# Kernel tuning notes

Hardware: AMD Instinct MI355X
Metric: run time of the kernel (lower is better)

The kernel has to match this reference:

```python
import jax, jax.numpy as jnp
import numpy as np

# ---------- filter construction (setup-time, numpy) ----------

def _conv2full(A, B):
    out = np.zeros((A.shape[0] + B.shape[0] - 1, A.shape[1] + B.shape[1] - 1))
    for i in range(B.shape[0]):
        for j in range(B.shape[1]):
            out[i:i + A.shape[0], j:j + A.shape[1]] += B[i, j] * A
    return out

def _mctrans(b, t):
    # McClellan transform of 1-D zero-phase filter b through kernel t
    n = (len(b) - 1) // 2
    c = len(b) // 2
    a = np.concatenate([[b[c]], 2.0 * b[c + 1:]])
    P0 = np.array([[1.0]]); P1 = t
    h = a[1] * t
    h[t.shape[0] // 2, t.shape[1] // 2] += a[0]
    for i in range(2, n + 1):
        P2 = 2.0 * _conv2full(t, P1)
        off = ((P2.shape[0] - P0.shape[0]) // 2, (P2.shape[1] - P0.shape[1]) // 2)
        P2[off[0]:off[0] + P0.shape[0], off[1]:off[1] + P0.shape[1]] -= P0
        hn = a[i] * P2
        o2 = ((P2.shape[0] - h.shape[0]) // 2, (P2.shape[1] - h.shape[1]) // 2)
        hn[o2[0]:o2[0] + h.shape[0], o2[1]:o2[1] + h.shape[1]] += h
        h = hn; P0, P1 = P1, P2
    return h

def _make_filters():
    # pyramidal 'maxflat' 1-D analysis pair (pfilters-style), DC gain sqrt(2)
    k1 = 1.0 - np.sqrt(2.0); k2 = 1.0 / np.sqrt(2.0); k3 = k1; M1 = 1.0 / np.sqrt(2.0)
    hh = np.array([0.25 * k2 * k3, 0.5 * k2, 1.0 + 0.5 * k2 * k3]) * M1
    h = np.concatenate([hh, hh[-2::-1]]) * np.sqrt(2.0)          # 5 taps
    gg = np.array([-0.125 * k1 * k2 * k3, 0.25 * k1 * k2,
                   -0.5 * k1 - 0.5 * k3 - 0.375 * k1 * k2 * k3,
                   1.0 + 0.5 * k1 * k2]) * M1
    g = np.concatenate([gg, gg[-2::-1]]) * np.sqrt(2.0)          # 7 taps
    # diamond maxflat lowpass via McClellan transform of Lagrange halfband
    b = np.array([-1., 0., 9., 16., 9., 0., -1.]) / 32.0
    t = np.array([[0., .25, 0.], [.25, 0., .25], [0., .25, 0.]])
    d0 = _mctrans(b, t)                                           # 7x7 diamond LP
    kh, kw = d0.shape
    mm = (-1.0) ** (np.add.outer(np.arange(kh) - kh // 2, np.arange(kw) - kw // 2))
    d1 = d0 * mm                                                  # complementary diamond
    colmod = (-1.0) ** (np.arange(kw) - kw // 2)                  # diamond -> fan
    f0 = d0 * colmod * np.sqrt(2.0)
    f1 = d1 * colmod * np.sqrt(2.0)
    return h, g, f0, f1

# ---------- jax filtering / resampling primitives ----------

def _sepfilt_per(x, f):
    # separable zero-phase filtering with periodic extension; x [B,C,H,W]
    B, C, H, W = x.shape
    L = f.shape[0]; p = L // 2
    k = f.astype(x.dtype)
    y = jnp.pad(x, ((0, 0), (0, 0), (p, p), (0, 0)), mode='wrap').reshape(B * C, 1, H + 2 * p, W)
    y = jax.lax.conv_general_dilated(y, k.reshape(1, 1, L, 1), (1, 1), 'VALID')
    y = jnp.pad(y, ((0, 0), (0, 0), (0, 0), (p, p)), mode='wrap')
    y = jax.lax.conv_general_dilated(y, k.reshape(1, 1, 1, L), (1, 1), 'VALID')
    return y.reshape(B, C, H, W)

def _filt2_per(x, F):
    B, C, H, W = x.shape
    kh, kw = F.shape; ph, pw = kh // 2, kw // 2
    y = jnp.pad(x, ((0, 0), (0, 0), (ph, ph), (pw, pw)), mode='wrap').reshape(B * C, 1, H + 2 * ph, W + 2 * pw)
    y = jax.lax.conv_general_dilated(y, F.reshape(1, 1, kh, kw).astype(x.dtype), (1, 1), 'VALID')
    return y.reshape(B, C, H, W)

def _qdown_r(x):
    # quincunx downsample: periodic row-shear then keep even rows -> [.., H/2, W]
    H, W = x.shape[-2], x.shape[-1]
    idx = (jnp.arange(W)[None, :] + jnp.arange(H)[:, None]) % W
    z = jnp.take_along_axis(x, jnp.broadcast_to(idx, x.shape), axis=-1)
    return z[..., ::2, :]

def _qdown_c(x):
    # quincunx downsample: periodic column-shear then keep even cols -> [.., H, W/2]
    H, W = x.shape[-2], x.shape[-1]
    idx = (jnp.arange(H)[:, None] + jnp.arange(W)[None, :]) % H
    z = jnp.take_along_axis(x, jnp.broadcast_to(idx, x.shape), axis=-2)
    return z[..., ::2]

# ---------- harness entry points ----------

def setup_inputs() -> dict:
    key = jax.random.key(0)
    x = jax.random.normal(key, (8, 96, 256, 256), dtype=jnp.float32)
    h, g, f0, f1 = _make_filters()
    return {
        'x': x,
        'h': jnp.asarray(h, dtype=jnp.float32),
        'g': jnp.asarray(g, dtype=jnp.float32),
        'f0': jnp.asarray(f0, dtype=jnp.float32),
        'f1': jnp.asarray(f1, dtype=jnp.float32),
    }

def reference(x, h, g, f0, f1):
    # pdfbdec with nlevs=[0,2]: one Laplacian-pyramid level + 2-level DFB on highpass
    xf = _sepfilt_per(x, h)
    xlo = xf[:, :, ::2, ::2]                                  # [B,C,H/2,W/2]
    up = jnp.zeros_like(x).at[:, :, ::2, ::2].set(xlo)
    xhi = x - _sepfilt_per(up, g)                             # LP bandpass [B,C,H,W]
    # DFB level 1: fan filters + quincunx ('1r')
    y0 = _qdown_r(_filt2_per(xhi, f0))                        # [B,C,H/2,W]
    y1 = _qdown_r(_filt2_per(xhi, f1))
    # DFB level 2: transposed fans + quincunx ('2c')
    subs = []
    for y in (y0, y1):
        subs.append(_qdown_c(_filt2_per(y, f0.T)))            # [B,C,H/2,W/2]
        subs.append(_qdown_c(_filt2_per(y, f1.T)))
    xhi_dir = jnp.stack(subs, axis=2)                         # [B,C,4,H/2,W/2]
    return xlo, xhi_dir
```

## Files before the change

kernel.cpp:

```cpp
#include <hip/hip_runtime.h>


#define BC 768

__global__ __launch_bounds__(256) void k1_lowpass(
    const float* __restrict__ x, const float* __restrict__ h,
    float* __restrict__ xlo)
{
    __shared__ float hs[5];
    int t = threadIdx.x;
    if (t < 5) hs[t] = h[t];
    __syncthreads();

    int tid = blockIdx.x * 256 + t;
    int cb = tid & 63;
    int rb = (tid >> 6) & 63;
    int bc = tid >> 12;
    const float* xb = x + (size_t)bc * 65536;

    int colp[4];
    #pragma unroll
    for (int k = 0; k < 4; ++k) colp[k] = (4 * cb - 2 + 2 * k) & 255;

    float a00 = 0.f, a01 = 0.f, a10 = 0.f, a11 = 0.f;
    #pragma unroll
    for (int pr = 0; pr < 7; ++pr) {
        int row = (4 * rb - 2 + pr) & 255;
        const float* xr = xb + row * 256;
        float X[8];
        #pragma unroll
        for (int k = 0; k < 4; ++k) {
            float2 p = *(const float2*)(xr + colp[k]);
            X[2 * k] = p.x; X[2 * k + 1] = p.y;
        }
        float s0 = hs[0]*X[0] + hs[1]*X[1] + hs[2]*X[2] + hs[3]*X[3] + hs[4]*X[4];
        float s1 = hs[0]*X[2] + hs[1]*X[3] + hs[2]*X[4] + hs[3]*X[5] + hs[4]*X[6];
        if (pr <= 4) { a00 += hs[pr] * s0;     a01 += hs[pr] * s1; }
        if (pr >= 2) { a10 += hs[pr - 2] * s0; a11 += hs[pr - 2] * s1; }
    }
    size_t ob = (size_t)bc * 16384 + (size_t)(2 * rb) * 128 + 2 * cb;
    *(float2*)(xlo + ob)       = make_float2(a00, a01);
    *(float2*)(xlo + ob + 128) = make_float2(a10, a11);
}

__global__ __launch_bounds__(256) void k2_highpass(
    const float* __restrict__ x, const float* __restrict__ g,
    const float* __restrict__ xlo, float* __restrict__ xs)
{
    __shared__ float gs[7];
    int t = threadIdx.x;
    if (t < 7) gs[t] = g[t];
    __syncthreads();

    int tid = blockIdx.x * 256 + t;
    int ch = tid & 127;
    int rh = (tid >> 7) & 127;
    int bc = tid >> 14;
    const float* lob = xlo + (size_t)bc * 16384;

    int ri[4] = { (rh - 1) & 127, rh, (rh + 1) & 127, (rh + 2) & 127 };
    int ci[4] = { (ch - 1) & 127, ch, (ch + 1) & 127, (ch + 2) & 127 };

    float ce[4], co[4];
    #pragma unroll
    for (int a = 0; a < 4; ++a) {
        const float* lr = lob + ri[a] * 128;
        float L0 = lr[ci[0]], L1 = lr[ci[1]], L2 = lr[ci[2]], L3 = lr[ci[3]];
        ce[a] = gs[1]*L0 + gs[3]*L1 + gs[5]*L2;
        co[a] = gs[0]*L0 + gs[2]*L1 + gs[4]*L2 + gs[6]*L3;
    }
    float aee = gs[1]*ce[0] + gs[3]*ce[1] + gs[5]*ce[2];
    float aeo = gs[1]*co[0] + gs[3]*co[1] + gs[5]*co[2];
    float aoe = gs[0]*ce[0] + gs[2]*ce[1] + gs[4]*ce[2] + gs[6]*ce[3];
    float aoo = gs[0]*co[0] + gs[2]*co[1] + gs[4]*co[2] + gs[6]*co[3];

    size_t base = (size_t)bc * 65536 + (size_t)(2 * rh) * 256 + 2 * ch;
    float2 xe = *(const float2*)(x + base);
    float2 xo = *(const float2*)(x + base + 256);

    float* xsb = (float*)xs + (size_t)bc * 65536;
    int re = 2 * rh, ro = 2 * rh + 1;
    int ce0 = (2 * ch - re + 2) & 255;
    int co0 = (2 * ch - ro + 2) & 255;
    *(float2*)(xsb + re * 256 + ce0) = make_float2(xe.x - aee, xe.y - aeo);
    float* rowo = xsb + ro * 256;
    rowo[co0]             = xo.x - aoe;
    rowo[(co0 + 1) & 255] = xo.y - aoo;
}

__global__ __launch_bounds__(256) void k3_dirfilt(
    const float* __restrict__ xs, const float* __restrict__ f0,
    const float* __restrict__ f1, float* __restrict__ y0,
    float* __restrict__ y1)
{
    __shared__ float F0[49], F1[49];
    int t = threadIdx.x;
    if (t < 49) F0[t] = f0[t];
    else if (t < 98) F1[t - 49] = f1[t - 49];
    __syncthreads();

    int wb = t & 63;
    int rg = t >> 6;
    int r0 = (blockIdx.x & 15) * 8;
    int bc = blockIdx.x >> 4;
    const float* xsb = xs + (size_t)bc * 65536;

    int base = 2 * r0 + 4 * rg - 3;
    int c0 = (4 * wb - 4) & 255;

    float a0[2][4] = {{0.f,0.f,0.f,0.f},{0.f,0.f,0.f,0.f}};
    float a1[2][4] = {{0.f,0.f,0.f,0.f},{0.f,0.f,0.f,0.f}};

    #pragma unroll
    for (int ro = 0; ro < 9; ++ro) {
        int row = (base + ro) & 255;
        const float* rp = xsb + row * 256;
        float C[16];
        #pragma unroll
        for (int k = 0; k < 4; ++k) {
            float4 v = *(const float4*)(rp + ((c0 + 4 * k) & 255));
            C[4*k] = v.x; C[4*k+1] = v.y; C[4*k+2] = v.z; C[4*k+3] = v.w;
        }
        #pragma unroll
        for (int lr = 0; lr < 2; ++lr) {
            int i = ro - 2 * lr;
            if (i >= 0 && i <= 6) {
                #pragma unroll
                for (int j = 0; j < 7; ++j) {
                    float w0 = F0[i * 7 + j];
                    float w1 = F1[i * 7 + j];
                    int mb = j - ro + 2 * lr + 6;
                    #pragma unroll
                    for (int dw = 0; dw < 4; ++dw) {
                        float v = C[dw + mb];
                        a0[lr][dw] += w0 * v;
                        a1[lr][dw] += w1 * v;
                    }
                }
            }
        }
    }
    #pragma unroll
    for (int lr = 0; lr < 2; ++lr) {
        int r = r0 + 2 * rg + lr;
        size_t o = (size_t)bc * 32768 + (size_t)r * 256 + 4 * wb;
        *(float4*)(y0 + o) = make_float4(a0[lr][0], a0[lr][1], a0[lr][2], a0[lr][3]);
        *(float4*)(y1 + o) = make_float4(a1[lr][0], a1[lr][1], a1[lr][2], a1[lr][3]);
    }
}

#define TH 32
#define TC 32
#define NR (TH + 2 * TC + 4)
#define NC (2 * TC + 6)
#define NCP 80

__global__ __launch_bounds__(256) void k4_qdc(
    const float* __restrict__ ybuf, const float* __restrict__ f0,
    const float* __restrict__ f1, float* __restrict__ out_hi)
{
    __shared__ float tile[NR * NCP];
    __shared__ float F0[49], F1[49];
    int t = threadIdx.x;
    if (t < 49) F0[t] = f0[t];
    else if (t < 98) F1[t - 49] = f1[t - 49];

    int bx   = blockIdx.x;
    int ccb  = (bx & 3) * TC;
    int hhb  = ((bx >> 2) & 3) * TH;
    int yidx = (bx >> 4) & 1;
    int bc   = bx >> 5;
    const float* yb = ybuf + ((size_t)yidx * BC + bc) * 32768;

    int r0 = (hhb + 2 * ccb - 3 + 128) & 127;
    int c0 = (2 * ccb - 3 + 256) & 255;

    for (int idx = t; idx < NR * NC; idx += 256) {
        int rr = idx / NC;
        int cc = idx - rr * NC;
        int gr = (r0 + rr) & 127;
        int gc = (c0 + cc) & 255;
        tile[rr * NCP + cc] = yb[gr * 256 + gc];
    }
    __syncthreads();

    int lc = t & 31;
    int lh = t >> 5;
    int cc = ccb + lc;
    int cbase = 2 * lc;
    int rbase0 = 4 * lh + 2 * lc;

    float s0[4] = {0.f, 0.f, 0.f, 0.f};
    float s1[4] = {0.f, 0.f, 0.f, 0.f};
    #pragma unroll
    for (int RR = 0; RR < 10; ++RR) {
        const float* tr = &tile[(rbase0 + RR) * NCP + cbase];
        float T[8];
        #pragma unroll
        for (int k = 0; k < 4; ++k) {
            float2 u = *(const float2*)(tr + 2 * k);
            T[2*k] = u.x; T[2*k+1] = u.y;
        }
        #pragma unroll
        for (int k = 0; k < 4; ++k) {
            int i = RR - k;
            if (i >= 0 && i <= 6) {
                #pragma unroll
                for (int j = 0; j < 7; ++j) {
                    s0[k] += F0[j * 7 + i] * T[j];
                    s1[k] += F1[j * 7 + i] * T[j];
                }
            }
        }
    }
    #pragma unroll
    for (int k = 0; k < 4; ++k) {
        int hh = hhb + 4 * lh + k;
        size_t o = (size_t)bc * 65536 + (size_t)(2 * yidx) * 16384
                 + (size_t)hh * 128 + cc;
        out_hi[o]         = s0[k];
        out_hi[o + 16384] = s1[k];
    }
}

extern "C" void kernel_launch(void* const* d_in, const int* in_sizes, int n_in,
                              void* d_out, int out_size, void* d_ws, size_t ws_size,
                              hipStream_t stream)
{
    const float* x  = (const float*)d_in[0];
    const float* h  = (const float*)d_in[1];
    const float* g  = (const float*)d_in[2];
    const float* f0 = (const float*)d_in[3];
    const float* f1 = (const float*)d_in[4];

    float* out   = (float*)d_out;
    float* xlo   = out;
    float* hireg = out + 12582912;
    float* ybuf  = (float*)d_ws;

    k1_lowpass<<<12288, 256, 0, stream>>>(x, h, xlo);
    k2_highpass<<<49152, 256, 0, stream>>>(x, g, xlo, hireg);
    k3_dirfilt<<<12288, 256, 0, stream>>>(hireg, f0, f1, ybuf, ybuf + 25165824);
    k4_qdc<<<24576, 256, 0, stream>>>(ybuf, f0, f1, hireg);
}
```

Baseline: 813.5 us.

## Load full-height strip per block in qdc kernel and read filter taps directly

```diff
diff --git a/kernel.cpp b/kernel.cpp
--- a/kernel.cpp
+++ b/kernel.cpp
@@ -7,11 +7,7 @@
     const float* __restrict__ x, const float* __restrict__ h,
     float* __restrict__ xlo)
 {
-    __shared__ float hs[5];
-    int t = threadIdx.x;
-    if (t < 5) hs[t] = h[t];
-    __syncthreads();
-
+    int t = threadIdx.x;
     int tid = blockIdx.x * 256 + t;
     int cb = tid & 63;
     int rb = (tid >> 6) & 63;
@@ -33,10 +29,10 @@
             float2 p = *(const float2*)(xr + colp[k]);
             X[2 * k] = p.x; X[2 * k + 1] = p.y;
         }
-        float s0 = hs[0]*X[0] + hs[1]*X[1] + hs[2]*X[2] + hs[3]*X[3] + hs[4]*X[4];
-        float s1 = hs[0]*X[2] + hs[1]*X[3] + hs[2]*X[4] + hs[3]*X[5] + hs[4]*X[6];
-        if (pr <= 4) { a00 += hs[pr] * s0;     a01 += hs[pr] * s1; }
-        if (pr >= 2) { a10 += hs[pr - 2] * s0; a11 += hs[pr - 2] * s1; }
+        float s0 = h[0]*X[0] + h[1]*X[1] + h[2]*X[2] + h[3]*X[3] + h[4]*X[4];
+        float s1 = h[0]*X[2] + h[1]*X[3] + h[2]*X[4] + h[3]*X[5] + h[4]*X[6];
+        if (pr <= 4) { a00 += h[pr] * s0;     a01 += h[pr] * s1; }
+        if (pr >= 2) { a10 += h[pr - 2] * s0; a11 += h[pr - 2] * s1; }
     }
     size_t ob = (size_t)bc * 16384 + (size_t)(2 * rb) * 128 + 2 * cb;
     *(float2*)(xlo + ob)       = make_float2(a00, a01);
@@ -47,11 +43,7 @@
     const float* __restrict__ x, const float* __restrict__ g,
     const float* __restrict__ xlo, float* __restrict__ xs)
 {
-    __shared__ float gs[7];
-    int t = threadIdx.x;
-    if (t < 7) gs[t] = g[t];
-    __syncthreads();
-
+    int t = threadIdx.x;
     int tid = blockIdx.x * 256 + t;
     int ch = tid & 127;
     int rh = (tid >> 7) & 127;
@@ -66,19 +58,19 @@
     for (int a = 0; a < 4; ++a) {
         const float* lr = lob + ri[a] * 128;
         float L0 = lr[ci[0]], L1 = lr[ci[1]], L2 = lr[ci[2]], L3 = lr[ci[3]];
-        ce[a] = gs[1]*L0 + gs[3]*L1 + gs[5]*L2;
-        co[a] = gs[0]*L0 + gs[2]*L1 + gs[4]*L2 + gs[6]*L3;
-    }
-    float aee = gs[1]*ce[0] + gs[3]*ce[1] + gs[5]*ce[2];
-    float aeo = gs[1]*co[0] + gs[3]*co[1] + gs[5]*co[2];
-    float aoe = gs[0]*ce[0] + gs[2]*ce[1] + gs[4]*ce[2] + gs[6]*ce[3];
-    float aoo = gs[0]*co[0] + gs[2]*co[1] + gs[4]*co[2] + gs[6]*co[3];
+        ce[a] = g[1]*L0 + g[3]*L1 + g[5]*L2;
+        co[a] = g[0]*L0 + g[2]*L1 + g[4]*L2 + g[6]*L3;
+    }
+    float aee = g[1]*ce[0] + g[3]*ce[1] + g[5]*ce[2];
+    float aeo = g[1]*co[0] + g[3]*co[1] + g[5]*co[2];
+    float aoe = g[0]*ce[0] + g[2]*ce[1] + g[4]*ce[2] + g[6]*ce[3];
+    float aoo = g[0]*co[0] + g[2]*co[1] + g[4]*co[2] + g[6]*co[3];
 
     size_t base = (size_t)bc * 65536 + (size_t)(2 * rh) * 256 + 2 * ch;
     float2 xe = *(const float2*)(x + base);
     float2 xo = *(const float2*)(x + base + 256);
 
-    float* xsb = (float*)xs + (size_t)bc * 65536;
+    float* xsb = xs + (size_t)bc * 65536;
     int re = 2 * rh, ro = 2 * rh + 1;
     int ce0 = (2 * ch - re + 2) & 255;
     int co0 = (2 * ch - ro + 2) & 255;
@@ -93,12 +85,7 @@
     const float* __restrict__ f1, float* __restrict__ y0,
     float* __restrict__ y1)
 {
-    __shared__ float F0[49], F1[49];
-    int t = threadIdx.x;
-    if (t < 49) F0[t] = f0[t];
-    else if (t < 98) F1[t - 49] = f1[t - 49];
-    __syncthreads();
-
+    int t = threadIdx.x;
     int wb = t & 63;
     int rg = t >> 6;
     int r0 = (blockIdx.x & 15) * 8;
@@ -127,8 +114,8 @@
             if (i >= 0 && i <= 6) {
                 #pragma unroll
                 for (int j = 0; j < 7; ++j) {
-                    float w0 = F0[i * 7 + j];
-                    float w1 = F1[i * 7 + j];
+                    float w0 = f0[i * 7 + j];
+                    float w1 = f1[i * 7 + j];
                     int mb = j - ro + 2 * lr + 6;
                     #pragma unroll
                     for (int dw = 0; dw < 4; ++dw) {
@@ -149,38 +136,27 @@
     }
 }
 
-#define TH 32
-#define TC 32
-#define NR (TH + 2 * TC + 4)
-#define NC (2 * TC + 6)
 #define NCP 80
 
 __global__ __launch_bounds__(256) void k4_qdc(
     const float* __restrict__ ybuf, const float* __restrict__ f0,
     const float* __restrict__ f1, float* __restrict__ out_hi)
 {
-    __shared__ float tile[NR * NCP];
-    __shared__ float F0[49], F1[49];
-    int t = threadIdx.x;
-    if (t < 49) F0[t] = f0[t];
-    else if (t < 98) F1[t - 49] = f1[t - 49];
+    __shared__ float tile[128 * NCP];
+    int t = threadIdx.x;
 
     int bx   = blockIdx.x;
-    int ccb  = (bx & 3) * TC;
-    int hhb  = ((bx >> 2) & 3) * TH;
-    int yidx = (bx >> 4) & 1;
-    int bc   = bx >> 5;
+    int ccb  = (bx & 3) * 32;
+    int yidx = (bx >> 2) & 1;
+    int bc   = bx >> 3;
     const float* yb = ybuf + ((size_t)yidx * BC + bc) * 32768;
 
-    int r0 = (hhb + 2 * ccb - 3 + 128) & 127;
     int c0 = (2 * ccb - 3 + 256) & 255;
 
-    for (int idx = t; idx < NR * NC; idx += 256) {
-        int rr = idx / NC;
-        int cc = idx - rr * NC;
-        int gr = (r0 + rr) & 127;
-        int gc = (c0 + cc) & 255;
-        tile[rr * NCP + cc] = yb[gr * 256 + gc];
+    for (int idx = t; idx < 128 * 70; idx += 256) {
+        int rr = idx / 70;
+        int cc = idx - rr * 70;
+        tile[rr * NCP + cc] = yb[rr * 256 + ((c0 + cc) & 255)];
     }
     __syncthreads();
 
@@ -188,13 +164,15 @@
     int lh = t >> 5;
     int cc = ccb + lc;
     int cbase = 2 * lc;
-    int rbase0 = 4 * lh + 2 * lc;
-
-    float s0[4] = {0.f, 0.f, 0.f, 0.f};
-    float s1[4] = {0.f, 0.f, 0.f, 0.f};
-    #pragma unroll
-    for (int RR = 0; RR < 10; ++RR) {
-        const float* tr = &tile[(rbase0 + RR) * NCP + cbase];
+    int rbase = (16 * lh + 2 * cc - 3 + 128) & 127;
+
+    float s0[16], s1[16];
+    #pragma unroll
+    for (int m = 0; m < 16; ++m) { s0[m] = 0.f; s1[m] = 0.f; }
+
+    #pragma unroll
+    for (int RR = 0; RR < 22; ++RR) {
+        const float* tr = &tile[((rbase + RR) & 127) * NCP + cbase];
         float T[8];
         #pragma unroll
         for (int k = 0; k < 4; ++k) {
@@ -202,24 +180,24 @@
             T[2*k] = u.x; T[2*k+1] = u.y;
         }
         #pragma unroll
-        for (int k = 0; k < 4; ++k) {
-            int i = RR - k;
+        for (int m = 0; m < 16; ++m) {
+            int i = RR - m;
             if (i >= 0 && i <= 6) {
                 #pragma unroll
                 for (int j = 0; j < 7; ++j) {
-                    s0[k] += F0[j * 7 + i] * T[j];
-                    s1[k] += F1[j * 7 + i] * T[j];
+                    s0[m] += f0[j * 7 + i] * T[j];
+                    s1[m] += f1[j * 7 + i] * T[j];
                 }
             }
         }
     }
     #pragma unroll
-    for (int k = 0; k < 4; ++k) {
-        int hh = hhb + 4 * lh + k;
+    for (int m = 0; m < 16; ++m) {
+        int hh = 16 * lh + m;
         size_t o = (size_t)bc * 65536 + (size_t)(2 * yidx) * 16384
                  + (size_t)hh * 128 + cc;
-        out_hi[o]         = s0[k];
-        out_hi[o + 16384] = s1[k];
+        out_hi[o]         = s0[m];
+        out_hi[o + 16384] = s1[m];
     }
 }
 
@@ -241,5 +219,5 @@
     k1_lowpass<<<12288, 256, 0, stream>>>(x, h, xlo);
     k2_highpass<<<49152, 256, 0, stream>>>(x, g, xlo, hireg);
     k3_dirfilt<<<12288, 256, 0, stream>>>(hireg, f0, f1, ybuf, ybuf + 25165824);
-    k4_qdc<<<24576, 256, 0, stream>>>(ybuf, f0, f1, hireg);
-}
+    k4_qdc<<<6144, 256, 0, stream>>>(ybuf, f0, f1, hireg);
+}
```

New measurement: 716.2 us. -12.0%, faster.
